# Kernel tuning notes

Measured on AMD Instinct MI355X. Metric: run time of the kernel, lower is better.

The kernel has to match this reference:

```python
import jax, jax.numpy as jnp
import numpy as np

N_NODES = 100000
N_EDGES = 1600000
D_IN = 128
D_HID = 128
D_OUT = 64


def setup_inputs() -> dict:
    key = jax.random.key(0)
    ks = jax.random.split(key, 8)
    x = jax.random.normal(ks[0], (N_NODES, D_IN), dtype=jnp.float32)
    edge_index = jax.random.randint(ks[1], (2, N_EDGES), 0, N_NODES, dtype=jnp.int64)
    s1 = 1.0 / np.sqrt(D_IN)
    s2 = 1.0 / np.sqrt(D_HID)
    W1 = jax.random.uniform(ks[2], (D_IN, D_HID), jnp.float32, -s1, s1)
    b1 = jnp.zeros((D_HID,), jnp.float32)
    W2 = jax.random.uniform(ks[3], (D_HID, D_HID), jnp.float32, -s2, s2)
    b2 = jnp.zeros((D_HID,), jnp.float32)
    fc_W = jax.random.uniform(ks[4], (D_HID, D_OUT), jnp.float32, -s2, s2)
    fc_b = jax.random.uniform(ks[5], (D_OUT,), jnp.float32, -s2, s2)
    return {"x": x, "edge_index": edge_index, "W1": W1, "b1": b1,
            "W2": W2, "b2": b2, "fc_W": fc_W, "fc_b": fc_b}


def _gcn_norm(edge_index, n_nodes):
    # add self-loops, compute symmetric normalization D^{-1/2} A D^{-1/2}
    loops = jnp.arange(n_nodes, dtype=edge_index.dtype)
    src = jnp.concatenate([edge_index[0], loops])  # [E+N]
    dst = jnp.concatenate([edge_index[1], loops])
    ones = jnp.ones(src.shape[0], jnp.float32)
    deg = jax.ops.segment_sum(ones, dst, num_segments=n_nodes)  # [N]
    dinv = 1.0 / jnp.sqrt(deg)  # deg >= 1 thanks to self-loops
    norm = dinv[src] * dinv[dst]  # [E+N]
    return src, dst, norm


def _gcn_conv(x, W, b, src, dst, norm, n_nodes):
    h = x @ W                                  # [N, d]
    msg = h[src] * norm[:, None]               # gather + scale, [E+N, d]
    out = jax.ops.segment_sum(msg, dst, num_segments=n_nodes)  # scatter-add
    return out + b


def reference(x, edge_index, W1, b1, W2, b2, fc_W, fc_b):
    n = x.shape[0]
    src, dst, norm = _gcn_norm(edge_index, n)
    h = jax.nn.relu(_gcn_conv(x, W1, b1, src, dst, norm, n))
    # dropout is identity in inference mode
    h = jax.nn.relu(_gcn_conv(h, W2, b2, src, dst, norm, n))
    return h @ fc_W + fc_b
```

## Files before the change

kernel.cpp:

```cpp
#include <hip/hip_runtime.h>

typedef __attribute__((ext_vector_type(8))) short bf16x8;
typedef __attribute__((ext_vector_type(4))) float f32x4;

__device__ __forceinline__ unsigned short f2bf(float x) {
  union { float f; unsigned u; } v; v.f = x;
  return (unsigned short)((v.u + 0x7fffu + ((v.u >> 16) & 1u)) >> 16);
}
__device__ __forceinline__ float bf2f(unsigned short h) {
  union { unsigned u; float f; } v; v.u = ((unsigned)h) << 16; return v.f;
}


__global__ __launch_bounds__(256) void bhist_k(const int* __restrict__ dst,
                                               int* __restrict__ bcnt, int E, int B) {
  __shared__ int h[512];
  for (int i = threadIdx.x; i < B; i += 256) h[i] = 0;
  __syncthreads();
  for (int e = blockIdx.x * 256 + threadIdx.x; e < E; e += gridDim.x * 256)
    atomicAdd(&h[dst[e] >> 8], 1);
  __syncthreads();
  for (int i = threadIdx.x; i < B; i += 256)
    if (h[i]) atomicAdd(&bcnt[i * 16], h[i]);
}

__global__ __launch_bounds__(512) void bscan_k(const int* __restrict__ bcnt,
                                               int* __restrict__ bstart,
                                               int* __restrict__ bfill,
                                               int* __restrict__ row_start,
                                               int B, int N, int E) {
  __shared__ int sd[512];
  int t = threadIdx.x;
  int v = (t < B) ? bcnt[t * 16] : 0;
  sd[t] = v; __syncthreads();
  for (int off = 1; off < 512; off <<= 1) {
    int x = (t >= off) ? sd[t - off] : 0;
    __syncthreads();
    sd[t] += x;
    __syncthreads();
  }
  if (t < B) {
    int excl = sd[t] - v;
    bstart[t] = excl;
    bfill[t * 16] = excl;
  }
  if (t == 0) { bstart[B] = E; row_start[N] = E; }
}

__global__ __launch_bounds__(256) void bin_k(const int* __restrict__ src,
                                             const int* __restrict__ dst,
                                             int* __restrict__ bfill,
                                             unsigned* __restrict__ ebuf, int E, int B) {
  __shared__ int hist[512];
  __shared__ int base[512];
  int t = threadIdx.x;
  int chunk = (E + gridDim.x - 1) / gridDim.x;
  int e0 = blockIdx.x * chunk;
  int e1 = e0 + chunk; if (e1 > E) e1 = E;
  for (int i = t; i < B; i += 256) hist[i] = 0;
  __syncthreads();
  for (int e = e0 + t; e < e1; e += 256) atomicAdd(&hist[dst[e] >> 8], 1);
  __syncthreads();
  for (int i = t; i < B; i += 256) {
    int c = hist[i];
    base[i] = c ? atomicAdd(&bfill[i * 16], c) : 0;
  }
  __syncthreads();
  for (int e = e0 + t; e < e1; e += 256) {
    int d = dst[e];
    int b = d >> 8;
    int pos = atomicAdd(&base[b], 1);
    ebuf[pos] = ((unsigned)(d & 255) << 17) | (unsigned)src[e];
  }
}

__global__ __launch_bounds__(256) void bsort_k(const unsigned* __restrict__ ebuf,
                                               const int* __restrict__ bstart,
                                               int* __restrict__ csr,
                                               int* __restrict__ row_start,
                                               float* __restrict__ dinv, int N) {
  __shared__ int cnt[256];
  __shared__ int sd[256];
  __shared__ int ofs[256];
  __shared__ int sorted[8192];
  int b = blockIdx.x, t = threadIdx.x;
  int bs = bstart[b], be = bstart[b + 1];
  int m = be - bs;
  if (m > 8192) m = 8192;
  cnt[t] = 0;
  __syncthreads();
  for (int i = t; i < m; i += 256) atomicAdd(&cnt[ebuf[bs + i] >> 17], 1);
  __syncthreads();
  int deg = cnt[t];
  sd[t] = deg; __syncthreads();
  for (int off = 1; off < 256; off <<= 1) {
    int x = (t >= off) ? sd[t - off] : 0;
    __syncthreads();
    sd[t] += x;
    __syncthreads();
  }
  int excl = sd[t] - deg;
  ofs[t] = excl;
  int node = (b << 8) + t;
  if (node < N) {
    row_start[node] = bs + excl;
    dinv[node] = rsqrtf((float)(deg + 1));
  }
  __syncthreads();
  for (int i = t; i < m; i += 256) {
    unsigned r = ebuf[bs + i];
    int d = r >> 17;
    int p = atomicAdd(&ofs[d], 1);
    if (p < 8192) sorted[p] = (int)(r & 0x1FFFFu);
  }
  __syncthreads();
  for (int i = t; i < m; i += 256) csr[bs + i] = sorted[i];
}

template <int NCOL, bool INF32, bool OUTF32>
__global__ __launch_bounds__(256) void gemm_k(const void* __restrict__ Ap,
                                              const float* __restrict__ W,
                                              const float* __restrict__ bias,
                                              void* __restrict__ Cp, int M) {
  __shared__ __align__(16) unsigned short Ws[NCOL * 136];
  int tid = threadIdx.x;
  for (int e = tid; e < 128 * NCOL; e += 256) {
    int k = e / NCOL, n = e % NCOL;
    Ws[n * 136 + k] = f2bf(W[e]);
  }
  __syncthreads();

  int wave = tid >> 6, lane = tid & 63;
  int q = lane >> 4, r = lane & 15;
  const int NT = NCOL / 16;
  int ntile = M >> 4;
  for (int tile = blockIdx.x * 4 + wave; tile < ntile; tile += gridDim.x * 4) {
    int row = tile * 16 + r;
    bf16x8 a[4];
    if (INF32) {
      const float* A = (const float*)Ap + (size_t)row * 128 + q * 8;
#pragma unroll
      for (int kk = 0; kk < 4; kk++) {
        const float4* p = (const float4*)(A + kk * 32);
        float4 f0 = p[0], f1 = p[1];
        bf16x8 tt;
        tt[0] = (short)f2bf(f0.x); tt[1] = (short)f2bf(f0.y);
        tt[2] = (short)f2bf(f0.z); tt[3] = (short)f2bf(f0.w);
        tt[4] = (short)f2bf(f1.x); tt[5] = (short)f2bf(f1.y);
        tt[6] = (short)f2bf(f1.z); tt[7] = (short)f2bf(f1.w);
        a[kk] = tt;
      }
    } else {
      const unsigned short* A = (const unsigned short*)Ap + (size_t)row * 128 + q * 8;
#pragma unroll
      for (int kk = 0; kk < 4; kk++) a[kk] = *(const bf16x8*)(A + kk * 32);
    }
    f32x4 acc[NT];
#pragma unroll
    for (int nt = 0; nt < NT; nt++) { acc[nt][0] = 0.f; acc[nt][1] = 0.f; acc[nt][2] = 0.f; acc[nt][3] = 0.f; }
#pragma unroll
    for (int kk = 0; kk < 4; kk++) {
#pragma unroll
      for (int nt = 0; nt < NT; nt++) {
        bf16x8 bfr = *(const bf16x8*)&Ws[(nt * 16 + r) * 136 + kk * 32 + q * 8];
        acc[nt] = __builtin_amdgcn_mfma_f32_16x16x32_bf16(a[kk], bfr, acc[nt], 0, 0, 0);
      }
    }
#pragma unroll
    for (int nt = 0; nt < NT; nt++) {
#pragma unroll
      for (int rr = 0; rr < 4; rr++) {
        int orow = tile * 16 + q * 4 + rr;
        int ocol = nt * 16 + r;
        if (OUTF32)
          ((float*)Cp)[(size_t)orow * NCOL + ocol] = acc[nt][rr] + bias[ocol];
        else
          ((unsigned short*)Cp)[(size_t)orow * NCOL + ocol] = f2bf(acc[nt][rr]);
      }
    }
  }
}

__global__ __launch_bounds__(256) void agg_k(const unsigned short* __restrict__ h,
                                             const float* __restrict__ dinv,
                                             const int* __restrict__ row_start,
                                             const int* __restrict__ csr,
                                             const float* __restrict__ bias,
                                             unsigned short* __restrict__ out, int N) {
  int lane = threadIdx.x & 63;
  int node = (blockIdx.x * 256 + threadIdx.x) >> 6;
  if (node >= N) return;
  int g = lane >> 4, r = lane & 15;
  float di = dinv[node];
  int beg = row_start[node];
  int deg = row_start[node + 1] - beg;

  float acc[8];
#pragma unroll
  for (int i = 0; i < 8; i++) acc[i] = 0.f;

  for (int base = -1; base < deg; base += 64) {
    int idx = base + lane;
    int s = node; float wv = 0.f;
    if (idx < 0) { wv = di; }
    else if (idx < deg) { s = csr[beg + idx]; wv = dinv[s]; }
    int cntv = deg - base; if (cntv > 64) cntv = 64;
    for (int j = 0; j < cntv; j += 4) {
      int lanesel = j + g;
      int sj = __shfl(s, lanesel);
      float wj = __shfl(wv, lanesel);
      bf16x8 hv = *(const bf16x8*)(h + (size_t)sj * 128 + r * 8);
#pragma unroll
      for (int i = 0; i < 8; i++)
        acc[i] += bf2f((unsigned short)hv[i]) * wj;
    }
  }

#pragma unroll
  for (int i = 0; i < 8; i++) {
    acc[i] += __shfl_xor(acc[i], 16);
    acc[i] += __shfl_xor(acc[i], 32);
  }

  if (g == 0) {
    bf16x8 t;
#pragma unroll
    for (int i = 0; i < 8; i++) {
      float v = acc[i] * di + bias[r * 8 + i];
      if (v < 0.f) v = 0.f;
      t[i] = (short)f2bf(v);
    }
    *(bf16x8*)(out + (size_t)node * 128 + r * 8) = t;
  }
}

extern "C" void kernel_launch(void* const* d_in, const int* in_sizes, int n_in,
                              void* d_out, int out_size, void* d_ws, size_t ws_size,
                              hipStream_t stream) {
  const float* x  = (const float*)d_in[0];
  const int* ei   = (const int*)d_in[1];
  const float* W1 = (const float*)d_in[2];
  const float* b1 = (const float*)d_in[3];
  const float* W2 = (const float*)d_in[4];
  const float* b2 = (const float*)d_in[5];
  const float* fcW = (const float*)d_in[6];
  const float* fcb = (const float*)d_in[7];
  float* out = (float*)d_out;

  int N = in_sizes[0] / 128;
  int E = in_sizes[1] / 2;
  int B = (N + 255) >> 8;
  const int* src = ei;
  const int* dst = ei + E;

  char* w = (char*)d_ws;
  auto alloc = [&](size_t b) { char* p = w; w += (b + 255) & ~(size_t)255; return p; };
  float* dinv      = (float*)alloc((size_t)N * 4);
  int*   row_start = (int*)alloc((size_t)(N + 1) * 4);
  int*   bcnt      = (int*)alloc((size_t)(B + 1) * 64);
  int*   bstart    = (int*)alloc((size_t)(B + 1) * 4);
  int*   bfill     = (int*)alloc((size_t)(B + 1) * 64);
  unsigned* ebuf   = (unsigned*)alloc((size_t)E * 4);
  int*   csr       = (int*)alloc((size_t)E * 4);
  unsigned short* bufA = (unsigned short*)alloc((size_t)N * 128 * 2);
  unsigned short* bufB = (unsigned short*)alloc((size_t)N * 128 * 2);

  hipMemsetAsync(bcnt, 0, (size_t)(B + 1) * 64, stream);

  bhist_k<<<256, 256, 0, stream>>>(dst, bcnt, E, B);
  bscan_k<<<1, 512, 0, stream>>>(bcnt, bstart, bfill, row_start, B, N, E);
  bin_k<<<256, 256, 0, stream>>>(src, dst, bfill, ebuf, E, B);
  bsort_k<<<B, 256, 0, stream>>>(ebuf, bstart, csr, row_start, dinv, N);

  gemm_k<128, true, false><<<512, 256, 0, stream>>>((const void*)x, W1, nullptr, (void*)bufA, N);
  agg_k<<<(N + 3) / 4, 256, 0, stream>>>(bufA, dinv, row_start, csr, b1, bufB, N);
  gemm_k<128, false, false><<<512, 256, 0, stream>>>((const void*)bufB, W2, nullptr, (void*)bufA, N);
  agg_k<<<(N + 3) / 4, 256, 0, stream>>>(bufA, dinv, row_start, csr, b2, bufB, N);
  gemm_k<64, false, true><<<512, 256, 0, stream>>>((const void*)bufB, fcW, fcb, (void*)out, N);
}
```

Measured before the change: 336.8 us.

## Fuse aggregation with following GEMM and precompute packed source/weight edge records

Replaces the separate aggregation and GEMM kernels with a fused kernel. Each block aggregates 64 nodes into a shared-memory tile, then multiplies that tile by the next weight matrix with MFMA, so the intermediate feature matrix never goes through global memory. It also adds a pass that packs each CSR source index together with its dinv value into an int2, which removes the dependent dinv gather during aggregation. In exchange, every block reconverts the weights into LDS, the edge array doubles in size, and each wave processes 16 nodes one after another, which may lower parallelism and latency hiding in the gather phase.

```diff
diff --git a/kernel.cpp b/kernel.cpp
--- a/kernel.cpp
+++ b/kernel.cpp
@@ -117,6 +117,16 @@
   for (int i = t; i < m; i += 256) csr[bs + i] = sorted[i];
 }
 
+__global__ __launch_bounds__(256) void wfill_k(const int* __restrict__ csr,
+                                               const float* __restrict__ dinv,
+                                               int2* __restrict__ csrw, int E) {
+  int e = blockIdx.x * 256 + threadIdx.x;
+  if (e < E) {
+    int s = csr[e];
+    csrw[e] = make_int2(s, __float_as_int(dinv[s]));
+  }
+}
+
 template <int NCOL, bool INF32, bool OUTF32>
 __global__ __launch_bounds__(256) void gemm_k(const void* __restrict__ Ap,
                                               const float* __restrict__ W,
@@ -181,56 +191,98 @@
   }
 }
 
-__global__ __launch_bounds__(256) void agg_k(const unsigned short* __restrict__ h,
-                                             const float* __restrict__ dinv,
-                                             const int* __restrict__ row_start,
-                                             const int* __restrict__ csr,
-                                             const float* __restrict__ bias,
-                                             unsigned short* __restrict__ out, int N) {
-  int lane = threadIdx.x & 63;
-  int node = (blockIdx.x * 256 + threadIdx.x) >> 6;
-  if (node >= N) return;
+template <int NCOL, bool OUTF32>
+__global__ __launch_bounds__(256) void aggmm_k(const unsigned short* __restrict__ h,
+                                               const int2* __restrict__ csrw,
+                                               const int* __restrict__ row_start,
+                                               const float* __restrict__ dinv,
+                                               const float* __restrict__ bias_agg,
+                                               const float* __restrict__ W,
+                                               const float* __restrict__ bias_out,
+                                               void* __restrict__ out, int N) {
+  __shared__ __align__(16) unsigned short Ws[NCOL * 136];
+  __shared__ __align__(16) unsigned short Hs[64 * 136];
+  int tid = threadIdx.x;
+  for (int e = tid; e < 128 * NCOL; e += 256) {
+    int k = e / NCOL, n = e % NCOL;
+    Ws[n * 136 + k] = f2bf(W[e]);
+  }
+  __syncthreads();
+
+  int wave = tid >> 6, lane = tid & 63;
   int g = lane >> 4, r = lane & 15;
-  float di = dinv[node];
-  int beg = row_start[node];
-  int deg = row_start[node + 1] - beg;
-
-  float acc[8];
-#pragma unroll
-  for (int i = 0; i < 8; i++) acc[i] = 0.f;
-
-  for (int base = -1; base < deg; base += 64) {
-    int idx = base + lane;
-    int s = node; float wv = 0.f;
-    if (idx < 0) { wv = di; }
-    else if (idx < deg) { s = csr[beg + idx]; wv = dinv[s]; }
-    int cntv = deg - base; if (cntv > 64) cntv = 64;
-    for (int j = 0; j < cntv; j += 4) {
-      int lanesel = j + g;
-      int sj = __shfl(s, lanesel);
-      float wj = __shfl(wv, lanesel);
-      bf16x8 hv = *(const bf16x8*)(h + (size_t)sj * 128 + r * 8);
-#pragma unroll
-      for (int i = 0; i < 8; i++)
-        acc[i] += bf2f((unsigned short)hv[i]) * wj;
-    }
-  }
-
-#pragma unroll
-  for (int i = 0; i < 8; i++) {
-    acc[i] += __shfl_xor(acc[i], 16);
-    acc[i] += __shfl_xor(acc[i], 32);
-  }
-
-  if (g == 0) {
-    bf16x8 t;
-#pragma unroll
-    for (int i = 0; i < 8; i++) {
-      float v = acc[i] * di + bias[r * 8 + i];
-      if (v < 0.f) v = 0.f;
-      t[i] = (short)f2bf(v);
-    }
-    *(bf16x8*)(out + (size_t)node * 128 + r * 8) = t;
+  int tile0 = blockIdx.x * 64;
+
+  for (int i = 0; i < 16; ++i) {
+    int node = tile0 + wave * 16 + i;
+    if (node >= N) break;
+    float di = dinv[node];
+    int beg = row_start[node];
+    int deg = row_start[node + 1] - beg;
+    float acc[8];
+#pragma unroll
+    for (int t = 0; t < 8; t++) acc[t] = 0.f;
+    for (int base = -1; base < deg; base += 64) {
+      int idx = base + lane;
+      int s = node; float wv = 0.f;
+      if (idx < 0) { wv = di; }
+      else if (idx < deg) {
+        int2 rec = csrw[beg + idx];
+        s = rec.x; wv = __int_as_float(rec.y);
+      }
+      int cntv = deg - base; if (cntv > 64) cntv = 64;
+      for (int j = 0; j < cntv; j += 4) {
+        int sj = __shfl(s, j + g);
+        float wj = __shfl(wv, j + g);
+        bf16x8 hv = *(const bf16x8*)(h + (size_t)sj * 128 + r * 8);
+#pragma unroll
+        for (int t = 0; t < 8; t++) acc[t] += bf2f((unsigned short)hv[t]) * wj;
+      }
+    }
+#pragma unroll
+    for (int t = 0; t < 8; t++) {
+      acc[t] += __shfl_xor(acc[t], 16);
+      acc[t] += __shfl_xor(acc[t], 32);
+    }
+    if (g == 0) {
+      bf16x8 tv;
+#pragma unroll
+      for (int t = 0; t < 8; t++) {
+        float v = acc[t] * di + bias_agg[r * 8 + t];
+        if (v < 0.f) v = 0.f;
+        tv[t] = (short)f2bf(v);
+      }
+      *(bf16x8*)&Hs[(wave * 16 + i) * 136 + r * 8] = tv;
+    }
+  }
+
+  const int NT = NCOL / 16;
+  int q = g;
+  f32x4 accv[NT];
+#pragma unroll
+  for (int nt = 0; nt < NT; nt++) { accv[nt][0] = 0.f; accv[nt][1] = 0.f; accv[nt][2] = 0.f; accv[nt][3] = 0.f; }
+#pragma unroll
+  for (int kk = 0; kk < 4; kk++) {
+    bf16x8 af = *(const bf16x8*)&Hs[(wave * 16 + r) * 136 + kk * 32 + q * 8];
+#pragma unroll
+    for (int nt = 0; nt < NT; nt++) {
+      bf16x8 bfr = *(const bf16x8*)&Ws[(nt * 16 + r) * 136 + kk * 32 + q * 8];
+      accv[nt] = __builtin_amdgcn_mfma_f32_16x16x32_bf16(af, bfr, accv[nt], 0, 0, 0);
+    }
+  }
+#pragma unroll
+  for (int nt = 0; nt < NT; nt++) {
+#pragma unroll
+    for (int rr = 0; rr < 4; rr++) {
+      int orow = tile0 + wave * 16 + q * 4 + rr;
+      if (orow < N) {
+        int ocol = nt * 16 + r;
+        if (OUTF32)
+          ((float*)out)[(size_t)orow * NCOL + ocol] = accv[nt][rr] + bias_out[ocol];
+        else
+          ((unsigned short*)out)[(size_t)orow * NCOL + ocol] = f2bf(accv[nt][rr]);
+      }
+    }
   }
 }
 
@@ -262,6 +314,7 @@
   int*   bfill     = (int*)alloc((size_t)(B + 1) * 64);
   unsigned* ebuf   = (unsigned*)alloc((size_t)E * 4);
   int*   csr       = (int*)alloc((size_t)E * 4);
+  int2*  csrw      = (int2*)alloc((size_t)E * 8);
   unsigned short* bufA = (unsigned short*)alloc((size_t)N * 128 * 2);
   unsigned short* bufB = (unsigned short*)alloc((size_t)N * 128 * 2);
 
@@ -271,10 +324,11 @@
   bscan_k<<<1, 512, 0, stream>>>(bcnt, bstart, bfill, row_start, B, N, E);
   bin_k<<<256, 256, 0, stream>>>(src, dst, bfill, ebuf, E, B);
   bsort_k<<<B, 256, 0, stream>>>(ebuf, bstart, csr, row_start, dinv, N);
+  wfill_k<<<(E + 255) / 256, 256, 0, stream>>>(csr, dinv, csrw, E);
 
   gemm_k<128, true, false><<<512, 256, 0, stream>>>((const void*)x, W1, nullptr, (void*)bufA, N);
-  agg_k<<<(N + 3) / 4, 256, 0, stream>>>(bufA, dinv, row_start, csr, b1, bufB, N);
-  gemm_k<128, false, false><<<512, 256, 0, stream>>>((const void*)bufB, W2, nullptr, (void*)bufA, N);
-  agg_k<<<(N + 3) / 4, 256, 0, stream>>>(bufA, dinv, row_start, csr, b2, bufB, N);
-  gemm_k<64, false, true><<<512, 256, 0, stream>>>((const void*)bufB, fcW, fcb, (void*)out, N);
-}
+  aggmm_k<128, false><<<(N + 63) / 64, 256, 0, stream>>>(bufA, csrw, row_start, dinv, b1, W2,
+                                                         nullptr, (void*)bufB, N);
+  aggmm_k<64, true><<<(N + 63) / 64, 256, 0, stream>>>(bufB, csrw, row_start, dinv, b2, fcW,
+                                                       fcb, (void*)out, N);
+}
```

New measurement: 464.4 us. 37.9% more time.
